# Performance work log

Measured on AMD Instinct MI355X. Metric: run time of the kernel, lower is better.

The kernel has to match this reference:

```python
import jax, jax.numpy as jnp
import numpy as np

D_MODEL = 1024
N_HEADS = 16
HEAD_DIM = D_MODEL // N_HEADS


def setup_inputs() -> dict:
    key = jax.random.key(0)
    ks = jax.random.split(key, 9)
    s = 0.02
    return {
        "x": jax.random.normal(ks[0], (2, 2048, D_MODEL), jnp.float32),
        "Wk": jax.random.normal(ks[1], (D_MODEL, D_MODEL), jnp.float32) * s,
        "bk": jnp.zeros((D_MODEL,), jnp.float32),
        "Wq": jax.random.normal(ks[2], (D_MODEL, D_MODEL), jnp.float32) * s,
        "bq": jnp.zeros((D_MODEL,), jnp.float32),
        "Wv": jax.random.normal(ks[3], (D_MODEL, D_MODEL), jnp.float32) * s,
        "bv": jnp.zeros((D_MODEL,), jnp.float32),
        "Wp": jax.random.normal(ks[4], (D_MODEL, D_MODEL), jnp.float32) * s,
        "bp": jnp.zeros((D_MODEL,), jnp.float32),
    }


def reference(x, Wk, bk, Wq, bq, Wv, bv, Wp, bp):
    B, T, C = x.shape
    H, Dh = N_HEADS, HEAD_DIM
    # linear projections; torch Linear: y = x @ W.T + b
    def split_heads(y):
        return y.reshape(B, T, H, Dh).transpose(0, 2, 1, 3)  # [B,H,T,Dh]
    k = split_heads(x @ Wk.T + bk)
    q = split_heads(x @ Wq.T + bq)
    v = split_heads(x @ Wv.T + bv)
    scale = 1.0 / jnp.sqrt(jnp.asarray(Dh, x.dtype))
    att = jnp.einsum("bhqd,bhkd->bhqk", q, k) * scale  # [B,H,T,T]
    causal = jnp.tril(jnp.ones((T, T), bool))
    att = jnp.where(causal[None, None], att, -jnp.inf)
    att = jax.nn.softmax(att, axis=-1)
    y = jnp.einsum("bhqk,bhkd->bhqd", att, v)  # [B,H,T,Dh]
    y = y.transpose(0, 2, 1, 3).reshape(B, T, C)
    return y @ Wp.T + bp
```

## Files before the change

kernel.cpp:

```cpp
#include <hip/hip_runtime.h>
#include <stdint.h>

typedef unsigned short u16;
typedef __bf16 bf16x8_t __attribute__((ext_vector_type(8)));
typedef float f32x4 __attribute__((ext_vector_type(4)));

#define T_LEN 2048
#define NHEADS 16
#define DHEAD 64
#define DMODEL 1024
#define QSCALE 0.1803368801111f

__device__ __forceinline__ u16 f2bf(float f) {
  union { float f; uint32_t u; } v; v.f = f;
  uint32_t r = v.u + 0x7FFFu + ((v.u >> 16) & 1u);
  return (u16)(r >> 16);
}

__device__ __forceinline__ void gload16(const u16* g, u16* l) {
  __builtin_amdgcn_global_load_lds((const __attribute__((address_space(1))) void*)g,
                                   (__attribute__((address_space(3))) void*)l, 16, 0, 0);
}

__global__ void cvt_bf16_k(const float* __restrict__ s, u16* __restrict__ d, int n) {
  int i = (blockIdx.x * blockDim.x + threadIdx.x) * 4;
  if (i >= n) return;
  float4 f = *(const float4*)(s + i);
  u16 o[4] = { f2bf(f.x), f2bf(f.y), f2bf(f.z), f2bf(f.w) };
  *(uint2*)(d + i) = *(const uint2*)o;
}

__global__ void cvt_w_k(const float* __restrict__ wq, const float* __restrict__ wk,
                        const float* __restrict__ wv, const float* __restrict__ wp,
                        u16* __restrict__ dqkv, u16* __restrict__ dp) {
  int which = blockIdx.y;
  const float* s = which == 0 ? wq : (which == 1 ? wk : (which == 2 ? wv : wp));
  u16* d = which == 3 ? dp : dqkv + (size_t)which * 1048576;
  int i = (blockIdx.x * blockDim.x + threadIdx.x) * 4;
  float4 f = *(const float4*)(s + i);
  u16 o[4] = { f2bf(f.x), f2bf(f.y), f2bf(f.z), f2bf(f.w) };
  *(uint2*)(d + i) = *(const uint2*)o;
}

template <int TM, int TN, int MODE>
__global__ __launch_bounds__(256, 3) void gemm_k(
    const u16* __restrict__ A, const u16* __restrict__ Bw,
    const float* __restrict__ b0, const float* __restrict__ b1, const float* __restrict__ b2,
    void* __restrict__ o0, void* __restrict__ o1, void* __restrict__ o2,
    int M, int N, int K)
{
  __shared__ __align__(16) u16 As[TM][64];
  __shared__ __align__(16) u16 Bs[TN][64];
  const int m0 = blockIdx.x * TM, n0 = blockIdx.y * TN;
  const int tid = threadIdx.x, lane = tid & 63, w = tid >> 6;
  const int col = lane & 15, quad = lane >> 4;
  constexpr int WM = TM / 2, WN = TN / 2;
  const int wm = (w >> 1) * WM, wn = (w & 1) * WN;
  constexpr int NI = WM / 16, NJ = WN / 16;
  const int rsub = lane >> 3;
  const int csw = ((lane & 7) ^ rsub) * 8;
  const int rx8 = col & 7;

  f32x4 acc[NI][NJ] = {};

  for (int k0 = 0; k0 < K; k0 += 64) {
    __syncthreads();
#pragma unroll
    for (int i = 0; i < TM / 32; i++) {
      int rb = (i * 4 + w) * 8;
      gload16(&A[(size_t)(m0 + rb + rsub) * K + k0 + csw], &As[rb][0]);
    }
#pragma unroll
    for (int i = 0; i < TN / 32; i++) {
      int rb = (i * 4 + w) * 8;
      gload16(&Bw[(size_t)(n0 + rb + rsub) * K + k0 + csw], &Bs[rb][0]);
    }
    __syncthreads();
#pragma unroll
    for (int s = 0; s < 2; s++) {
      bf16x8_t af[NI], bfr[NJ];
#pragma unroll
      for (int i = 0; i < NI; i++) {
        int cp = (quad ^ rx8) ^ (s * 4);
        af[i] = *(const bf16x8_t*)&As[wm + i * 16 + col][cp * 8];
      }
#pragma unroll
      for (int j = 0; j < NJ; j++) {
        int cp = (quad ^ rx8) ^ (s * 4);
        bfr[j] = *(const bf16x8_t*)&Bs[wn + j * 16 + col][cp * 8];
      }
#pragma unroll
      for (int i = 0; i < NI; i++)
#pragma unroll
        for (int j = 0; j < NJ; j++)
          acc[i][j] = __builtin_amdgcn_mfma_f32_16x16x32_bf16(af[i], bfr[j], acc[i][j], 0, 0, 0);
    }
  }

#pragma unroll
  for (int i = 0; i < NI; i++) {
#pragma unroll
    for (int j = 0; j < NJ; j++) {
      int ncol = n0 + wn + j * 16 + col;
      if (MODE == 0) {
        float bias = b0[ncol];
#pragma unroll
        for (int r = 0; r < 4; r++) {
          int m = m0 + wm + i * 16 + quad * 4 + r;
          ((float*)o0)[(size_t)m * N + ncol] = acc[i][j][r] + bias;
        }
      } else {
        int sect = ncol >> 10, nc = ncol & 1023;
        const float* bp = sect == 0 ? b0 : (sect == 1 ? b1 : b2);
        u16* op = sect == 0 ? (u16*)o0 : (sect == 1 ? (u16*)o1 : (u16*)o2);
        float bias = bp[nc];
        float scal = sect == 0 ? QSCALE : 1.0f;
        int h = nc >> 6, d = nc & 63;
#pragma unroll
        for (int r = 0; r < 4; r++) {
          int m = m0 + wm + i * 16 + quad * 4 + r;
          int b = m >> 11, t = m & 2047;
          float v = (acc[i][j][r] + bias) * scal;
          size_t idx = sect < 2 ? ((((size_t)(b * NHEADS + h)) * T_LEN + t) * DHEAD + d)
                                : ((((size_t)(b * NHEADS + h)) * DHEAD + d) * T_LEN + t);
          op[idx] = f2bf(v);
        }
      }
    }
  }
}

__global__ __launch_bounds__(256, 4) void attn_k(
    const u16* __restrict__ Q, const u16* __restrict__ Kb,
    const u16* __restrict__ Vt, u16* __restrict__ Y)
{
  __shared__ __align__(16) u16 Ks[2][64][64];
  __shared__ __align__(16) u16 Vs[2][64][64];
  const int bid = blockIdx.x;
  const int bh = (bid & 7) * 4 + ((bid >> 3) & 3);
  const int qt = 31 - (bid >> 5);
  const int tid = threadIdx.x, lane = tid & 63, w = tid >> 6;
  const int col = lane & 15, quad = lane >> 4;
  const int b = bh >> 4, h = bh & 15;
  const int qw = qt * 64 + w * 16;

  const int rsub = lane >> 3;
  const int csw = ((lane & 7) ^ rsub) * 8;
  const u16* kgb = Kb + (size_t)bh * T_LEN * DHEAD;
  const u16* vgb = Vt + (size_t)bh * DHEAD * T_LEN;
  const int rx = col & 7;

  bf16x8_t qf0, qf1;
  {
    const u16* p = Q + ((size_t)bh * T_LEN + qw + col) * DHEAD + quad * 8;
    qf0 = *(const bf16x8_t*)p;
    qf1 = *(const bf16x8_t*)(p + 32);
  }

  const int qr = qw + col;
  float ls[4] = {0.f, 0.f, 0.f, 0.f};
  f32x4 o[4] = {};

#pragma unroll
  for (int half = 0; half < 2; half++) {
    int rb = w * 16 + half * 8;
    gload16(kgb + (size_t)(rb + rsub) * DHEAD + csw, &Ks[0][rb][0]);
    gload16(vgb + (size_t)(rb + rsub) * T_LEN + csw, &Vs[0][rb][0]);
  }

  for (int kt = 0; kt <= qt; ++kt) {
    const int k0 = kt * 64;
    const int bufi = kt & 1;
    __syncthreads();
    if (kt < qt) {
      const int k0n = k0 + 64, bn = bufi ^ 1;
#pragma unroll
      for (int half = 0; half < 2; half++) {
        int rb = w * 16 + half * 8;
        gload16(kgb + (size_t)(k0n + rb + rsub) * DHEAD + csw, &Ks[bn][rb][0]);
        gload16(vgb + (size_t)(rb + rsub) * T_LEN + k0n + csw, &Vs[bn][rb][0]);
      }
    }

    f32x4 s[4];
#pragma unroll
    for (int nt = 0; nt < 4; nt++) {
      const u16* krow = &Ks[bufi][nt * 16 + col][0];
      bf16x8_t kf0 = *(const bf16x8_t*)(krow + ((quad ^ rx) & 7) * 8);
      bf16x8_t kf1 = *(const bf16x8_t*)(krow + (((4 + quad) ^ rx) & 7) * 8);
      f32x4 a = {};
      a = __builtin_amdgcn_mfma_f32_16x16x32_bf16(kf0, qf0, a, 0, 0, 0);
      a = __builtin_amdgcn_mfma_f32_16x16x32_bf16(kf1, qf1, a, 0, 0, 0);
      s[nt] = a;
    }

    const bool diag = (kt == qt);
    u16 pb[4][4];
#pragma unroll
    for (int nt = 0; nt < 4; nt++) {
#pragma unroll
      for (int r = 0; r < 4; r++) {
        float p = __builtin_amdgcn_exp2f(s[nt][r]);
        if (diag && (k0 + nt * 16 + quad * 4 + r) > qr) p = 0.f;
        uint32_t pu = __float_as_uint(p) & 0xFFFF0000u;
        ls[r] += __uint_as_float(pu);
        pb[nt][r] = (u16)(pu >> 16);
      }
    }
    union PU { bf16x8_t v; u16 h[8]; } pf[2];
#pragma unroll
    for (int r = 0; r < 4; r++) {
      pf[0].h[r] = pb[0][r]; pf[0].h[4 + r] = pb[1][r];
      pf[1].h[r] = pb[2][r]; pf[1].h[4 + r] = pb[3][r];
    }

#pragma unroll
    for (int ks = 0; ks < 2; ks++) {
#pragma unroll
      for (int dt = 0; dt < 4; dt++) {
        const u16* vrow = &Vs[bufi][dt * 16 + col][0];
        union VU { bf16x8_t v; uint2 u2[2]; } va;
        va.u2[0] = *(const uint2*)(vrow + ((ks * 4 + (quad >> 1)) ^ rx) * 8 + (quad & 1) * 4);
        va.u2[1] = *(const uint2*)(vrow + ((ks * 4 + 2 + (quad >> 1)) ^ rx) * 8 + (quad & 1) * 4);
        o[dt] = __builtin_amdgcn_mfma_f32_16x16x32_bf16(va.v, pf[ks].v, o[dt], 0, 0, 0);
      }
    }
  }

  float lsum = (ls[0] + ls[1]) + (ls[2] + ls[3]);
  lsum += __shfl_xor(lsum, 16);
  lsum += __shfl_xor(lsum, 32);
  float inv = 1.0f / lsum;
  int t = qw + col;
#pragma unroll
  for (int dt = 0; dt < 4; dt++) {
    u16 w4[4];
#pragma unroll
    for (int r = 0; r < 4; r++) w4[r] = f2bf(o[dt][r] * inv);
    *(uint2*)&Y[((size_t)(b * T_LEN + t)) * DMODEL + h * DHEAD + dt * 16 + quad * 4] =
        *(const uint2*)w4;
  }
}

extern "C" void kernel_launch(void* const* d_in, const int* in_sizes, int n_in,
                              void* d_out, int out_size, void* d_ws, size_t ws_size,
                              hipStream_t stream) {
  const float* x  = (const float*)d_in[0];
  const float* Wk = (const float*)d_in[1];
  const float* bk = (const float*)d_in[2];
  const float* Wq = (const float*)d_in[3];
  const float* bq = (const float*)d_in[4];
  const float* Wv = (const float*)d_in[5];
  const float* bv = (const float*)d_in[6];
  const float* Wp = (const float*)d_in[7];
  const float* bp = (const float*)d_in[8];

  char* ws = (char*)d_ws;
  const size_t MB = 1u << 20;
  u16* xb    = (u16*)(ws);
  u16* wqkv  = (u16*)(ws + 8 * MB);
  u16* wpb   = (u16*)(ws + 14 * MB);
  u16* qb    = (u16*)(ws + 16 * MB);
  u16* kb    = (u16*)(ws + 24 * MB);
  u16* vtb   = (u16*)(ws + 32 * MB);
  u16* yatt  = (u16*)(ws + 40 * MB);

  cvt_bf16_k<<<4096, 256, 0, stream>>>(x, xb, 4194304);
  dim3 gw(1024, 4);
  cvt_w_k<<<gw, 256, 0, stream>>>(Wq, Wk, Wv, Wp, wqkv, wpb);

  dim3 gqkv(32, 24);
  gemm_k<128, 128, 3><<<gqkv, 256, 0, stream>>>(xb, wqkv, bq, bk, bv,
                                                qb, kb, vtb, 4096, 3072, 1024);

  attn_k<<<1024, 256, 0, stream>>>(qb, kb, vtb, yatt);

  dim3 gp(32, 16);
  gemm_k<128, 64, 0><<<gp, 256, 0, stream>>>(yatt, wpb, bp, nullptr, nullptr,
                                             d_out, nullptr, nullptr, 4096, 1024, 1024);
}
```

Before: 175.8 us.

## Process two query tiles per attention block to reuse K/V loads, merge convert kernels

The attention kernel now handles 128 query rows per block, as two 64-row sub-tiles sharing each staged K/V tile. This halves LDS fragment loads per MFMA, and the causal diagonal handling is specialised at compile time. It also adds s_setprio hints around the MFMA phases. The grid shrinks to 512 blocks with launch bounds lowered to 2, and the x and weight conversion kernels are merged into one launch. In exchange, register pressure rises and parallelism drops, which may leave CUs underused and worsen causal load imbalance.

```diff
diff --git a/kernel.cpp b/kernel.cpp
--- a/kernel.cpp
+++ b/kernel.cpp
@@ -11,6 +11,9 @@
 #define DMODEL 1024
 #define QSCALE 0.1803368801111f
 
+template <int N> struct IC { static constexpr int v = N; };
+union PU { bf16x8_t v; u16 h[8]; };
+
 __device__ __forceinline__ u16 f2bf(float f) {
   union { float f; uint32_t u; } v; v.f = f;
   uint32_t r = v.u + 0x7FFFu + ((v.u >> 16) & 1u);
@@ -22,21 +25,20 @@
                                    (__attribute__((address_space(3))) void*)l, 16, 0, 0);
 }
 
-__global__ void cvt_bf16_k(const float* __restrict__ s, u16* __restrict__ d, int n) {
-  int i = (blockIdx.x * blockDim.x + threadIdx.x) * 4;
-  if (i >= n) return;
-  float4 f = *(const float4*)(s + i);
-  u16 o[4] = { f2bf(f.x), f2bf(f.y), f2bf(f.z), f2bf(f.w) };
-  *(uint2*)(d + i) = *(const uint2*)o;
-}
-
-__global__ void cvt_w_k(const float* __restrict__ wq, const float* __restrict__ wk,
-                        const float* __restrict__ wv, const float* __restrict__ wp,
-                        u16* __restrict__ dqkv, u16* __restrict__ dp) {
-  int which = blockIdx.y;
-  const float* s = which == 0 ? wq : (which == 1 ? wk : (which == 2 ? wv : wp));
-  u16* d = which == 3 ? dp : dqkv + (size_t)which * 1048576;
-  int i = (blockIdx.x * blockDim.x + threadIdx.x) * 4;
+__global__ void cvt_all_k(const float* __restrict__ x,
+                          const float* __restrict__ wq, const float* __restrict__ wk,
+                          const float* __restrict__ wv, const float* __restrict__ wp,
+                          u16* __restrict__ xb, u16* __restrict__ dqkv, u16* __restrict__ dp) {
+  const float* s; u16* d; int i;
+  if (blockIdx.y == 0) {
+    s = x; d = xb;
+    i = (blockIdx.x * 256 + threadIdx.x) * 4;
+  } else {
+    int which = blockIdx.x >> 10;
+    s = which == 0 ? wq : (which == 1 ? wk : (which == 2 ? wv : wp));
+    d = which == 3 ? dp : dqkv + (size_t)which * 1048576;
+    i = (((blockIdx.x & 1023) * 256) + threadIdx.x) * 4;
+  }
   float4 f = *(const float4*)(s + i);
   u16 o[4] = { f2bf(f.x), f2bf(f.y), f2bf(f.z), f2bf(f.w) };
   *(uint2*)(d + i) = *(const uint2*)o;
@@ -130,7 +132,7 @@
   }
 }
 
-__global__ __launch_bounds__(256, 4) void attn_k(
+__global__ __launch_bounds__(256, 2) void attn_k(
     const u16* __restrict__ Q, const u16* __restrict__ Kb,
     const u16* __restrict__ Vt, u16* __restrict__ Y)
 {
@@ -138,11 +140,11 @@
   __shared__ __align__(16) u16 Vs[2][64][64];
   const int bid = blockIdx.x;
   const int bh = (bid & 7) * 4 + ((bid >> 3) & 3);
-  const int qt = 31 - (bid >> 5);
+  const int qt = 15 - (bid >> 5);
   const int tid = threadIdx.x, lane = tid & 63, w = tid >> 6;
   const int col = lane & 15, quad = lane >> 4;
   const int b = bh >> 4, h = bh & 15;
-  const int qw = qt * 64 + w * 16;
+  const int qw = qt * 128 + w * 16;
 
   const int rsub = lane >> 3;
   const int csw = ((lane & 7) ^ rsub) * 8;
@@ -150,70 +152,94 @@
   const u16* vgb = Vt + (size_t)bh * DHEAD * T_LEN;
   const int rx = col & 7;
 
-  bf16x8_t qf0, qf1;
+  bf16x8_t qf0a, qf0b, qf1a, qf1b;
   {
     const u16* p = Q + ((size_t)bh * T_LEN + qw + col) * DHEAD + quad * 8;
-    qf0 = *(const bf16x8_t*)p;
-    qf1 = *(const bf16x8_t*)(p + 32);
-  }
-
-  const int qr = qw + col;
-  float ls[4] = {0.f, 0.f, 0.f, 0.f};
-  f32x4 o[4] = {};
-
-#pragma unroll
-  for (int half = 0; half < 2; half++) {
-    int rb = w * 16 + half * 8;
-    gload16(kgb + (size_t)(rb + rsub) * DHEAD + csw, &Ks[0][rb][0]);
-    gload16(vgb + (size_t)(rb + rsub) * T_LEN + csw, &Vs[0][rb][0]);
-  }
-
-  for (int kt = 0; kt <= qt; ++kt) {
-    const int k0 = kt * 64;
-    const int bufi = kt & 1;
-    __syncthreads();
-    if (kt < qt) {
-      const int k0n = k0 + 64, bn = bufi ^ 1;
-#pragma unroll
-      for (int half = 0; half < 2; half++) {
-        int rb = w * 16 + half * 8;
-        gload16(kgb + (size_t)(k0n + rb + rsub) * DHEAD + csw, &Ks[bn][rb][0]);
-        gload16(vgb + (size_t)(rb + rsub) * T_LEN + k0n + csw, &Vs[bn][rb][0]);
-      }
-    }
-
-    f32x4 s[4];
+    qf0a = *(const bf16x8_t*)p;
+    qf0b = *(const bf16x8_t*)(p + 32);
+    const u16* p1 = p + (size_t)64 * DHEAD;
+    qf1a = *(const bf16x8_t*)p1;
+    qf1b = *(const bf16x8_t*)(p1 + 32);
+  }
+  const int qr0 = qw + col, qr1 = qw + 64 + col;
+
+  float ls0[4] = {0.f, 0.f, 0.f, 0.f}, ls1[4] = {0.f, 0.f, 0.f, 0.f};
+  f32x4 o0[4] = {}, o1[4] = {};
+
+  auto stage = [&](int ktile) {
+    const int k0n = ktile * 64, bufn = ktile & 1;
+#pragma unroll
+    for (int half = 0; half < 2; half++) {
+      int rb = w * 16 + half * 8;
+      gload16(kgb + (size_t)(k0n + rb + rsub) * DHEAD + csw, &Ks[bufn][rb][0]);
+      gload16(vgb + (size_t)(rb + rsub) * T_LEN + k0n + csw, &Vs[bufn][rb][0]);
+    }
+  };
+
+  auto tile = [&](int kt, auto M0c, auto M1c) {
+    constexpr int M0 = decltype(M0c)::v, M1 = decltype(M1c)::v;
+    const int k0 = kt * 64, bufi = kt & 1;
+    f32x4 s0[4], s1[4];
+    __builtin_amdgcn_s_setprio(1);
 #pragma unroll
     for (int nt = 0; nt < 4; nt++) {
       const u16* krow = &Ks[bufi][nt * 16 + col][0];
       bf16x8_t kf0 = *(const bf16x8_t*)(krow + ((quad ^ rx) & 7) * 8);
       bf16x8_t kf1 = *(const bf16x8_t*)(krow + (((4 + quad) ^ rx) & 7) * 8);
-      f32x4 a = {};
-      a = __builtin_amdgcn_mfma_f32_16x16x32_bf16(kf0, qf0, a, 0, 0, 0);
-      a = __builtin_amdgcn_mfma_f32_16x16x32_bf16(kf1, qf1, a, 0, 0, 0);
-      s[nt] = a;
-    }
-
-    const bool diag = (kt == qt);
-    u16 pb[4][4];
-#pragma unroll
-    for (int nt = 0; nt < 4; nt++) {
+      if (M0 != 2) {
+        f32x4 a = {};
+        a = __builtin_amdgcn_mfma_f32_16x16x32_bf16(kf0, qf0a, a, 0, 0, 0);
+        a = __builtin_amdgcn_mfma_f32_16x16x32_bf16(kf1, qf0b, a, 0, 0, 0);
+        s0[nt] = a;
+      }
+      if (M1 != 2) {
+        f32x4 a = {};
+        a = __builtin_amdgcn_mfma_f32_16x16x32_bf16(kf0, qf1a, a, 0, 0, 0);
+        a = __builtin_amdgcn_mfma_f32_16x16x32_bf16(kf1, qf1b, a, 0, 0, 0);
+        s1[nt] = a;
+      }
+    }
+    __builtin_amdgcn_s_setprio(0);
+
+    PU pf0[2], pf1[2];
+    if (M0 != 2) {
+      u16 pb[4][4];
+#pragma unroll
+      for (int nt = 0; nt < 4; nt++)
+#pragma unroll
+        for (int r = 0; r < 4; r++) {
+          float p = __builtin_amdgcn_exp2f(s0[nt][r]);
+          if (M0 == 1 && (k0 + nt * 16 + quad * 4 + r) > qr0) p = 0.f;
+          uint32_t pu = __float_as_uint(p) & 0xFFFF0000u;
+          ls0[r] += __uint_as_float(pu);
+          pb[nt][r] = (u16)(pu >> 16);
+        }
 #pragma unroll
       for (int r = 0; r < 4; r++) {
-        float p = __builtin_amdgcn_exp2f(s[nt][r]);
-        if (diag && (k0 + nt * 16 + quad * 4 + r) > qr) p = 0.f;
-        uint32_t pu = __float_as_uint(p) & 0xFFFF0000u;
-        ls[r] += __uint_as_float(pu);
-        pb[nt][r] = (u16)(pu >> 16);
-      }
-    }
-    union PU { bf16x8_t v; u16 h[8]; } pf[2];
-#pragma unroll
-    for (int r = 0; r < 4; r++) {
-      pf[0].h[r] = pb[0][r]; pf[0].h[4 + r] = pb[1][r];
-      pf[1].h[r] = pb[2][r]; pf[1].h[4 + r] = pb[3][r];
-    }
-
+        pf0[0].h[r] = pb[0][r]; pf0[0].h[4 + r] = pb[1][r];
+        pf0[1].h[r] = pb[2][r]; pf0[1].h[4 + r] = pb[3][r];
+      }
+    }
+    if (M1 != 2) {
+      u16 pb[4][4];
+#pragma unroll
+      for (int nt = 0; nt < 4; nt++)
+#pragma unroll
+        for (int r = 0; r < 4; r++) {
+          float p = __builtin_amdgcn_exp2f(s1[nt][r]);
+          if (M1 == 1 && (k0 + nt * 16 + quad * 4 + r) > qr1) p = 0.f;
+          uint32_t pu = __float_as_uint(p) & 0xFFFF0000u;
+          ls1[r] += __uint_as_float(pu);
+          pb[nt][r] = (u16)(pu >> 16);
+        }
+#pragma unroll
+      for (int r = 0; r < 4; r++) {
+        pf1[0].h[r] = pb[0][r]; pf1[0].h[4 + r] = pb[1][r];
+        pf1[1].h[r] = pb[2][r]; pf1[1].h[4 + r] = pb[3][r];
+      }
+    }
+
+    __builtin_amdgcn_s_setprio(1);
 #pragma unroll
     for (int ks = 0; ks < 2; ks++) {
 #pragma unroll
@@ -222,23 +248,56 @@
         union VU { bf16x8_t v; uint2 u2[2]; } va;
         va.u2[0] = *(const uint2*)(vrow + ((ks * 4 + (quad >> 1)) ^ rx) * 8 + (quad & 1) * 4);
         va.u2[1] = *(const uint2*)(vrow + ((ks * 4 + 2 + (quad >> 1)) ^ rx) * 8 + (quad & 1) * 4);
-        o[dt] = __builtin_amdgcn_mfma_f32_16x16x32_bf16(va.v, pf[ks].v, o[dt], 0, 0, 0);
-      }
-    }
-  }
-
-  float lsum = (ls[0] + ls[1]) + (ls[2] + ls[3]);
-  lsum += __shfl_xor(lsum, 16);
-  lsum += __shfl_xor(lsum, 32);
-  float inv = 1.0f / lsum;
-  int t = qw + col;
-#pragma unroll
-  for (int dt = 0; dt < 4; dt++) {
-    u16 w4[4];
-#pragma unroll
-    for (int r = 0; r < 4; r++) w4[r] = f2bf(o[dt][r] * inv);
-    *(uint2*)&Y[((size_t)(b * T_LEN + t)) * DMODEL + h * DHEAD + dt * 16 + quad * 4] =
-        *(const uint2*)w4;
+        if (M0 != 2) o0[dt] = __builtin_amdgcn_mfma_f32_16x16x32_bf16(va.v, pf0[ks].v, o0[dt], 0, 0, 0);
+        if (M1 != 2) o1[dt] = __builtin_amdgcn_mfma_f32_16x16x32_bf16(va.v, pf1[ks].v, o1[dt], 0, 0, 0);
+      }
+    }
+    __builtin_amdgcn_s_setprio(0);
+  };
+
+  stage(0);
+  int kt = 0;
+  for (; kt < 2 * qt; ++kt) {
+    __syncthreads();
+    stage(kt + 1);
+    tile(kt, IC<0>{}, IC<0>{});
+  }
+  __syncthreads();
+  stage(kt + 1);
+  tile(kt, IC<1>{}, IC<0>{});
+  ++kt;
+  __syncthreads();
+  tile(kt, IC<2>{}, IC<1>{});
+
+  {
+    float lsum = (ls0[0] + ls0[1]) + (ls0[2] + ls0[3]);
+    lsum += __shfl_xor(lsum, 16);
+    lsum += __shfl_xor(lsum, 32);
+    float inv = 1.0f / lsum;
+    int t = qw + col;
+#pragma unroll
+    for (int dt = 0; dt < 4; dt++) {
+      u16 w4[4];
+#pragma unroll
+      for (int r = 0; r < 4; r++) w4[r] = f2bf(o0[dt][r] * inv);
+      *(uint2*)&Y[((size_t)(b * T_LEN + t)) * DMODEL + h * DHEAD + dt * 16 + quad * 4] =
+          *(const uint2*)w4;
+    }
+  }
+  {
+    float lsum = (ls1[0] + ls1[1]) + (ls1[2] + ls1[3]);
+    lsum += __shfl_xor(lsum, 16);
+    lsum += __shfl_xor(lsum, 32);
+    float inv = 1.0f / lsum;
+    int t = qw + 64 + col;
+#pragma unroll
+    for (int dt = 0; dt < 4; dt++) {
+      u16 w4[4];
+#pragma unroll
+      for (int r = 0; r < 4; r++) w4[r] = f2bf(o1[dt][r] * inv);
+      *(uint2*)&Y[((size_t)(b * T_LEN + t)) * DMODEL + h * DHEAD + dt * 16 + quad * 4] =
+          *(const uint2*)w4;
+    }
   }
 }
 
@@ -265,15 +324,14 @@
   u16* vtb   = (u16*)(ws + 32 * MB);
   u16* yatt  = (u16*)(ws + 40 * MB);
 
-  cvt_bf16_k<<<4096, 256, 0, stream>>>(x, xb, 4194304);
-  dim3 gw(1024, 4);
-  cvt_w_k<<<gw, 256, 0, stream>>>(Wq, Wk, Wv, Wp, wqkv, wpb);
+  dim3 gcv(4096, 2);
+  cvt_all_k<<<gcv, 256, 0, stream>>>(x, Wq, Wk, Wv, Wp, xb, wqkv, wpb);
 
   dim3 gqkv(32, 24);
   gemm_k<128, 128, 3><<<gqkv, 256, 0, stream>>>(xb, wqkv, bq, bk, bv,
                                                 qb, kb, vtb, 4096, 3072, 1024);
 
-  attn_k<<<1024, 256, 0, stream>>>(qb, kb, vtb, yatt);
+  attn_k<<<512, 256, 0, stream>>>(qb, kb, vtb, yatt);
 
   dim3 gp(32, 16);
   gemm_k<128, 64, 0><<<gp, 256, 0, stream>>>(yatt, wpb, bp, nullptr, nullptr,
```

After: 185.9 us. +5.7%, slower.

## Use 256x256-tile double-buffered GEMM with XCD-aware block remap for QKV projection

Applied to the files above, without the earlier changes.

Adds a new GEMM kernel with 256x256 output tiles, 512 threads, double-buffered LDS staged via global_load_lds with XOR swizzle, and a block index remap that groups neighbouring tiles onto the same XCD. The QKV projection now uses it with 192 blocks instead of 768 128x128 blocks. The aim is higher arithmetic intensity and better L2 locality, fewer global loads per flop. The cost is 128 KB of LDS and heavy register use per block, which lowers occupancy, and 192 blocks may not fill all CUs evenly.

```diff
diff --git a/kernel.cpp b/kernel.cpp
--- a/kernel.cpp
+++ b/kernel.cpp
@@ -109,6 +109,81 @@
           int m = m0 + wm + i * 16 + quad * 4 + r;
           ((float*)o0)[(size_t)m * N + ncol] = acc[i][j][r] + bias;
         }
+      }
+    }
+  }
+}
+
+template <int MODE>
+__global__ __launch_bounds__(512, 2) void gemm256_k(
+    const u16* __restrict__ A, const u16* __restrict__ Bw,
+    const float* __restrict__ b0, const float* __restrict__ b1, const float* __restrict__ b2,
+    void* __restrict__ o0, void* __restrict__ o1, void* __restrict__ o2,
+    int M, int N, int K, int gx)
+{
+  __shared__ __align__(16) u16 As[2][256][64];
+  __shared__ __align__(16) u16 Bs[2][256][64];
+  const int nwg = gridDim.x;
+  const int cpx = nwg >> 3;
+  const int wg = (blockIdx.x & 7) * cpx + (blockIdx.x >> 3);
+  const int bx = wg % gx, by = wg / gx;
+  const int m0 = bx * 256, n0 = by * 256;
+  const int tid = threadIdx.x, lane = tid & 63, w = tid >> 6;
+  const int col = lane & 15, quad = lane >> 4;
+  const int wm = (w >> 2) * 128, wn = (w & 3) * 64;
+  const int rsub = lane >> 3;
+  const int csw = ((lane & 7) ^ rsub) * 8;
+  const int rx8 = col & 7;
+
+  f32x4 acc[8][4] = {};
+
+  auto stage = [&](int buf, int k0) {
+#pragma unroll
+    for (int i = 0; i < 4; i++) {
+      int rb = (i * 8 + w) * 8;
+      gload16(&A[(size_t)(m0 + rb + rsub) * K + k0 + csw], &As[buf][rb][0]);
+      gload16(&Bw[(size_t)(n0 + rb + rsub) * K + k0 + csw], &Bs[buf][rb][0]);
+    }
+  };
+
+  const int NT = K >> 6;
+  stage(0, 0);
+  __syncthreads();
+  int cur = 0;
+  for (int t = 0; t < NT; ++t) {
+    if (t + 1 < NT) stage(cur ^ 1, (t + 1) << 6);
+#pragma unroll
+    for (int s = 0; s < 2; s++) {
+      bf16x8_t af[8], bfr[4];
+      const int cp = ((quad ^ rx8) ^ (s * 4)) * 8;
+#pragma unroll
+      for (int i = 0; i < 8; i++)
+        af[i] = *(const bf16x8_t*)&As[cur][wm + i * 16 + col][cp];
+#pragma unroll
+      for (int j = 0; j < 4; j++)
+        bfr[j] = *(const bf16x8_t*)&Bs[cur][wn + j * 16 + col][cp];
+#pragma unroll
+      for (int i = 0; i < 8; i++)
+#pragma unroll
+        for (int j = 0; j < 4; j++)
+          acc[i][j] = __builtin_amdgcn_mfma_f32_16x16x32_bf16(af[i], bfr[j], acc[i][j], 0, 0, 0);
+    }
+    __syncthreads();
+    cur ^= 1;
+  }
+
+#pragma unroll
+  for (int i = 0; i < 8; i++) {
+#pragma unroll
+    for (int j = 0; j < 4; j++) {
+      int ncol = n0 + wn + j * 16 + col;
+      if (MODE == 0) {
+        float bias = b0[ncol];
+#pragma unroll
+        for (int r = 0; r < 4; r++) {
+          int m = m0 + wm + i * 16 + quad * 4 + r;
+          ((float*)o0)[(size_t)m * N + ncol] = acc[i][j][r] + bias;
+        }
       } else {
         int sect = ncol >> 10, nc = ncol & 1023;
         const float* bp = sect == 0 ? b0 : (sect == 1 ? b1 : b2);
@@ -269,9 +344,8 @@
   dim3 gw(1024, 4);
   cvt_w_k<<<gw, 256, 0, stream>>>(Wq, Wk, Wv, Wp, wqkv, wpb);
 
-  dim3 gqkv(32, 24);
-  gemm_k<128, 128, 3><<<gqkv, 256, 0, stream>>>(xb, wqkv, bq, bk, bv,
-                                                qb, kb, vtb, 4096, 3072, 1024);
+  gemm256_k<3><<<192, 512, 0, stream>>>(xb, wqkv, bq, bk, bv,
+                                        qb, kb, vtb, 4096, 3072, 1024, 16);
 
   attn_k<<<1024, 256, 0, stream>>>(qb, kb, vtb, yatt);
 
```

Measured after the change: 207.1 us. 17.8% more time.
